# Performance work log

Hardware: AMD Instinct MI355X
Metric: run time of the kernel (lower is better)

Reference implementation:

```python
import jax, jax.numpy as jnp
import numpy as np

DIM = 512
HEADS = 8
DHEAD = DIM // 8          # 64
INNER = HEADS * DHEAD     # 512
M_LANDMARKS = 256
PINV_ITERS = 6
KSZ = 33                  # residual depthwise conv kernel (default)


def setup_inputs() -> dict:
    key = jax.random.key(0)
    ks = jax.random.split(key, 5)
    B, N = 1, 16384
    s = DIM ** -0.5
    return {
        "x": jax.random.normal(ks[0], (B, N, DIM), jnp.float32),
        "norm_w": jnp.ones((DIM,), jnp.float32),
        "norm_b": jnp.zeros((DIM,), jnp.float32),
        "w_qkv": jax.random.normal(ks[1], (3 * INNER, DIM), jnp.float32) * s,   # Linear(dim, 3*inner, bias=False)
        "w_out": jax.random.normal(ks[2], (DIM, INNER), jnp.float32) * s,        # Linear(inner, dim)
        "b_out": jnp.zeros((DIM,), jnp.float32),
        "conv_w": jax.random.normal(ks[3], (HEADS, 1, KSZ, 1), jnp.float32) * 0.1,  # depthwise Conv2d(h,h,(33,1),groups=h)
    }


def _layernorm(x, w, b, eps=1e-5):
    mu = x.mean(-1, keepdims=True)
    var = ((x - mu) ** 2).mean(-1, keepdims=True)
    return (x - mu) * jax.lax.rsqrt(var + eps) * w + b


def _moore_penrose_pinv(a, iters):
    # a: [B, H, m, m]; matches lucidrains moore_penrose_iter_pinv (global max over col/row sums)
    abs_a = jnp.abs(a)
    col = abs_a.sum(-1).max()
    row = abs_a.sum(-2).max()
    z = jnp.swapaxes(a, -1, -2) / (col * row)
    I = jnp.eye(a.shape[-1], dtype=a.dtype)
    for _ in range(iters):
        az = a @ z
        z = 0.25 * z @ (13 * I - az @ (15 * I - az @ (7 * I - az)))
    return z


def _nystrom_attention(h, w_qkv, w_out, b_out, conv_w):
    B, N, _ = h.shape
    qkv = h @ w_qkv.T                          # [B, N, 3*inner]
    q, k, v = jnp.split(qkv, 3, axis=-1)

    def heads(t):
        return t.reshape(B, N, HEADS, DHEAD).transpose(0, 2, 1, 3)  # [B, H, N, d]
    q = heads(q) * (DHEAD ** -0.5)
    k = heads(k)
    v = heads(v)

    # landmark pooling: mean over contiguous groups of size l = N / m
    l = N // M_LANDMARKS
    q_l = q.reshape(B, HEADS, M_LANDMARKS, l, DHEAD).mean(3)   # [B, H, m, d]
    k_l = k.reshape(B, HEADS, M_LANDMARKS, l, DHEAD).mean(3)

    attn1 = jax.nn.softmax(jnp.einsum('bhnd,bhmd->bhnm', q, k_l), axis=-1)      # [B,H,N,m]
    attn2 = jax.nn.softmax(jnp.einsum('bhid,bhjd->bhij', q_l, k_l), axis=-1)    # [B,H,m,m]
    attn3 = jax.nn.softmax(jnp.einsum('bhmd,bhnd->bhmn', q_l, k), axis=-1)      # [B,H,m,N]

    attn2_inv = _moore_penrose_pinv(attn2, PINV_ITERS)
    out = attn1 @ (attn2_inv @ (attn3 @ v))                                     # [B,H,N,d]

    # residual depthwise conv along sequence dim (kernel 33x1, groups=HEADS, no bias)
    conv = jax.lax.conv_general_dilated(
        v, conv_w, window_strides=(1, 1),
        padding=((KSZ // 2, KSZ // 2), (0, 0)),
        dimension_numbers=('NCHW', 'OIHW', 'NCHW'),
        feature_group_count=HEADS)
    out = out + conv

    out = out.transpose(0, 2, 1, 3).reshape(B, N, INNER)
    return out @ w_out.T + b_out


def reference(x, norm_w, norm_b, w_qkv, w_out, b_out, conv_w):
    h = _layernorm(x, norm_w, norm_b)
    return x + _nystrom_attention(h, w_qkv, w_out, b_out, conv_w)
```

## Files before the change

### kernel.cpp

```cpp
#include <hip/hip_runtime.h>
#include <hip/hip_bf16.h>


typedef __attribute__((ext_vector_type(8))) short bf16x8;
typedef __attribute__((ext_vector_type(4))) float f32x4;

#define MFMA16(A, B, C) __builtin_amdgcn_mfma_f32_16x16x32_bf16(A, B, C, 0, 0, 0)
#define GLD16(g, l) __builtin_amdgcn_global_load_lds( \
    (const __attribute__((address_space(1))) void*)(g), \
    (__attribute__((address_space(3))) void*)(l), 16, 0, 0)

static __device__ __forceinline__ unsigned short f2b(float f) {
  __hip_bfloat16 h = __float2bfloat16(f);
  return *reinterpret_cast<unsigned short*>(&h);
}
static __device__ __forceinline__ float b2f(unsigned short u) {
  return __uint_as_float(((unsigned)u) << 16);
}

#define FMA16(ACC, AV, BV) do { \
  ACC[0][0] += AV.x*BV.x; ACC[0][1] += AV.x*BV.y; ACC[0][2] += AV.x*BV.z; ACC[0][3] += AV.x*BV.w; \
  ACC[1][0] += AV.y*BV.x; ACC[1][1] += AV.y*BV.y; ACC[1][2] += AV.y*BV.z; ACC[1][3] += AV.y*BV.w; \
  ACC[2][0] += AV.z*BV.x; ACC[2][1] += AV.z*BV.y; ACC[2][2] += AV.z*BV.z; ACC[2][3] += AV.z*BV.w; \
  ACC[3][0] += AV.w*BV.x; ACC[3][1] += AV.w*BV.y; ACC[3][2] += AV.w*BV.z; ACC[3][3] += AV.w*BV.w; \
} while (0)

__global__ __launch_bounds__(128) void k_ln(const float* __restrict__ x,
    const float* __restrict__ w, const float* __restrict__ b, unsigned short* __restrict__ h) {
  const int row = blockIdx.x;
  const int t = threadIdx.x;
  const float4 xv = ((const float4*)(x + (size_t)row * 512))[t];
  float s  = xv.x + xv.y + xv.z + xv.w;
  float sq = xv.x*xv.x + xv.y*xv.y + xv.z*xv.z + xv.w*xv.w;
  #pragma unroll
  for (int o = 32; o > 0; o >>= 1) {
    s  += __shfl_down(s, o, 64);
    sq += __shfl_down(sq, o, 64);
  }
  __shared__ float ls[2], lq[2];
  if ((t & 63) == 0) { ls[t >> 6] = s; lq[t >> 6] = sq; }
  __syncthreads();
  s = ls[0] + ls[1]; sq = lq[0] + lq[1];
  const float mean = s * (1.0f / 512.0f);
  const float var  = sq * (1.0f / 512.0f) - mean * mean;
  const float rstd = rsqrtf(var + 1e-5f);
  const float4 wv = ((const float4*)w)[t];
  const float4 bv = ((const float4*)b)[t];
  ushort4 hv;
  hv.x = f2b((xv.x - mean) * rstd * wv.x + bv.x);
  hv.y = f2b((xv.y - mean) * rstd * wv.y + bv.y);
  hv.z = f2b((xv.z - mean) * rstd * wv.z + bv.z);
  hv.w = f2b((xv.w - mean) * rstd * wv.w + bv.w);
  ((ushort4*)(h + (size_t)row * 512))[t] = hv;
}

__global__ __launch_bounds__(256) void k_cvt(const float* __restrict__ src,
    unsigned short* __restrict__ dst, int n4) {
  const int i = blockIdx.x * 256 + threadIdx.x;
  if (i < n4) {
    const float4 f = ((const float4*)src)[i];
    ushort4 u;
    u.x = f2b(f.x); u.y = f2b(f.y); u.z = f2b(f.z); u.w = f2b(f.w);
    ((ushort4*)dst)[i] = u;
  }
}

__device__ __forceinline__ void stage_tile(const unsigned short* __restrict__ A,
    const unsigned short* __restrict__ B, unsigned short* lds,
    int m0, int n0, int k0, int tid) {
  #pragma unroll
  for (int c = 0; c < 2; ++c) {
    const int s = c * 512 + tid;
    const int grow = ((s >> 6) << 4) | (s & 15);
    const int chunk = (s >> 4) & 3;
    GLD16(A + (size_t)(m0 + grow) * 512 + k0 + chunk * 8, lds + s * 8);
    GLD16(B + (size_t)(n0 + grow) * 512 + k0 + chunk * 8, lds + 8192 + s * 8);
  }
}

__device__ __forceinline__ void compute_tile(const unsigned short* lds,
    f32x4 (&acc)[8][4], int wr, int wc, int quad, int l15) {
  bf16x8 a[8], b[4];
  #pragma unroll
  for (int i = 0; i < 8; ++i)
    a[i] = *(const bf16x8*)(lds + (size_t)((wr * 8 + i) * 64 + quad * 16 + l15) * 8);
  #pragma unroll
  for (int j = 0; j < 4; ++j)
    b[j] = *(const bf16x8*)(lds + 8192 + (size_t)((wc * 4 + j) * 64 + quad * 16 + l15) * 8);
  __builtin_amdgcn_s_setprio(1);
  #pragma unroll
  for (int i = 0; i < 8; ++i)
    #pragma unroll
    for (int j = 0; j < 4; ++j)
      acc[i][j] = MFMA16(a[i], b[j], acc[i][j]);
  __builtin_amdgcn_s_setprio(0);
}

#define GEMM256_PIPELINE(Aptr, Bptr, M0, N0)                                 \
  f32x4 acc[8][4];                                                           \
  _Pragma("unroll")                                                          \
  for (int i = 0; i < 8; ++i)                                                \
    _Pragma("unroll")                                                        \
    for (int j = 0; j < 4; ++j) acc[i][j] = (f32x4){0.f, 0.f, 0.f, 0.f};     \
  stage_tile(Aptr, Bptr, lds, M0, N0, 0, tid);                               \
  asm volatile("" ::: "memory");                                             \
  stage_tile(Aptr, Bptr, lds + 16384, M0, N0, 32, tid);                      \
  asm volatile("s_waitcnt vmcnt(4)" ::: "memory");                           \
  __builtin_amdgcn_s_barrier();                                              \
  {                                                                          \
    int cb = 0, sb = 2;                                                      \
    for (int t = 0; t < 14; ++t) {                                           \
      stage_tile(Aptr, Bptr, lds + sb * 16384, M0, N0, (t + 2) * 32, tid);   \
      compute_tile(lds + cb * 16384, acc, wr, wc, quad, l15);                \
      asm volatile("s_waitcnt vmcnt(4)" ::: "memory");                       \
      __builtin_amdgcn_s_barrier();                                          \
      cb = (cb == 2) ? 0 : cb + 1;                                           \
      sb = (sb == 2) ? 0 : sb + 1;                                           \
    }                                                                        \
    compute_tile(lds + cb * 16384, acc, wr, wc, quad, l15);                  \
    cb = (cb == 2) ? 0 : cb + 1;                                             \
    asm volatile("s_waitcnt vmcnt(0)" ::: "memory");                         \
    __builtin_amdgcn_s_barrier();                                            \
    compute_tile(lds + cb * 16384, acc, wr, wc, quad, l15);                  \
  }

__global__ __launch_bounds__(512, 2) void k_qkv2(const unsigned short* __restrict__ A,
    const unsigned short* __restrict__ B,
    unsigned short* __restrict__ qb, unsigned short* __restrict__ kb,
    unsigned short* __restrict__ vb) {
  __shared__ unsigned short lds[49152];
  const int tid = threadIdx.x;
  const int lane = tid & 63, w = tid >> 6;
  const int wr = w >> 2, wc = w & 3;
  const int quad = lane >> 4, l15 = lane & 15;
  const int bid = blockIdx.x;
  const int swz = (bid & 7) * 48 + (bid >> 3);
  const int by = swz / 6, bx = swz - by * 6;
  const int m0 = by * 256, n0 = bx * 256;

  GEMM256_PIPELINE(A, B, m0, n0)

  const int part = n0 >> 9;
  const int head = ((n0 & 511) >> 6) + wc;
  unsigned short* dst = (part == 0) ? qb : (part == 1) ? kb : vb;
  const float scale = (part == 0) ? 0.125f : 1.0f;
  unsigned short* dp = dst + (size_t)head * 16384 * 64;
  #pragma unroll
  for (int i = 0; i < 8; ++i) {
    const int rowb = m0 + wr * 128 + i * 16 + quad * 4;
    #pragma unroll
    for (int j = 0; j < 4; ++j) {
      const int dd = j * 16 + l15;
      #pragma unroll
      for (int r = 0; r < 4; ++r)
        dp[(size_t)(rowb + r) * 64 + dd] = f2b(acc[i][j][r] * scale);
    }
  }
}

__global__ __launch_bounds__(512, 2) void k_out2(const unsigned short* __restrict__ A,
    const unsigned short* __restrict__ B, const float* __restrict__ bias,
    const float* __restrict__ xres, float* __restrict__ out) {
  __shared__ unsigned short lds[49152];
  const int tid = threadIdx.x;
  const int lane = tid & 63, w = tid >> 6;
  const int wr = w >> 2, wc = w & 3;
  const int quad = lane >> 4, l15 = lane & 15;
  const int bid = blockIdx.x;
  const int swz = (bid & 7) * 16 + (bid >> 3);
  const int by = swz >> 1, bx = swz & 1;
  const int m0 = by * 256, n0 = bx * 256;

  GEMM256_PIPELINE(A, B, m0, n0)

  #pragma unroll
  for (int j = 0; j < 4; ++j) {
    const int col = n0 + wc * 64 + j * 16 + l15;
    const float bv = bias[col];
    #pragma unroll
    for (int i = 0; i < 8; ++i) {
      const int rowb = m0 + wr * 128 + i * 16 + quad * 4;
      #pragma unroll
      for (int r = 0; r < 4; ++r) {
        const size_t idx = (size_t)(rowb + r) * 512 + col;
        out[idx] = acc[i][j][r] + bv + xres[idx];
      }
    }
  }
}

__global__ __launch_bounds__(256) void k_tr(const unsigned short* __restrict__ v,
    unsigned short* __restrict__ vt) {
  __shared__ unsigned short T[64][72];
  const int t = threadIdx.x;
  const int n0 = blockIdx.x * 64, h = blockIdx.y;
  const int n = t >> 2, sg = (t & 3) * 16;
  const unsigned short* p = v + ((size_t)(h * 16384 + n0 + n)) * 64 + sg;
  #pragma unroll
  for (int i = 0; i < 16; i += 4) {
    const ushort4 u = *(const ushort4*)(p + i);
    T[sg + i + 0][n] = u.x; T[sg + i + 1][n] = u.y;
    T[sg + i + 2][n] = u.z; T[sg + i + 3][n] = u.w;
  }
  __syncthreads();
  const int d = t >> 2, so = (t & 3) * 16;
  unsigned short* q = vt + ((size_t)(h * 64 + d)) * 16384 + n0 + so;
  #pragma unroll
  for (int i = 0; i < 16; i += 4) {
    ushort4 u;
    u.x = T[d][so + i]; u.y = T[d][so + i + 1];
    u.z = T[d][so + i + 2]; u.w = T[d][so + i + 3];
    *(ushort4*)(q + i) = u;
  }
}

__global__ __launch_bounds__(256) void k_landmark(const unsigned short* __restrict__ qb,
    const unsigned short* __restrict__ kb, float* __restrict__ qlf,
    unsigned short* __restrict__ qlb, float* __restrict__ klf,
    unsigned short* __restrict__ klb) {
  const int t = threadIdx.x, d = t & 63, grp = t >> 6;
  const int m = blockIdx.x, h = blockIdx.y;
  const unsigned short* src = blockIdx.z ? kb : qb;
  const unsigned short* p = src + ((size_t)h * 16384 + m * 64 + grp * 16) * 64 + d;
  float s = 0.f;
  #pragma unroll
  for (int i = 0; i < 16; ++i) s += b2f(p[(size_t)i * 64]);
  __shared__ float red[4][64];
  red[grp][d] = s;
  __syncthreads();
  if (t < 64) {
    float v = (red[0][d] + red[1][d]) + (red[2][d] + red[3][d]);
    v *= (1.0f / 64.0f);
    const size_t oi = ((size_t)h * 256 + m) * 64 + d;
    if (blockIdx.z == 0) { qlf[oi] = v; qlb[oi] = f2b(v); }
    else                 { klf[oi] = v; klb[oi] = f2b(v); }
  }
}

__global__ __launch_bounds__(256) void k_attn2(const float* __restrict__ ql,
    const float* __restrict__ kl, float* __restrict__ a2, unsigned short* __restrict__ a2b) {
  const int i = blockIdx.x, h = blockIdx.y, j = threadIdx.x;
  __shared__ float qrow[64];
  __shared__ float wred[4];
  __shared__ float wsum[4];
  if (j < 64) qrow[j] = ql[((size_t)h * 256 + i) * 64 + j];
  __syncthreads();
  const float* kr = kl + ((size_t)h * 256 + j) * 64;
  float s = 0.f;
  #pragma unroll 8
  for (int d = 0; d < 64; ++d) s += qrow[d] * kr[d];
  float mx = s;
  #pragma unroll
  for (int o2 = 32; o2 > 0; o2 >>= 1) mx = fmaxf(mx, __shfl_xor(mx, o2, 64));
  if ((j & 63) == 0) wred[j >> 6] = mx;
  __syncthreads();
  mx = fmaxf(fmaxf(wred[0], wred[1]), fmaxf(wred[2], wred[3]));
  const float e = __expf(s - mx);
  float sm = e;
  #pragma unroll
  for (int o2 = 32; o2 > 0; o2 >>= 1) sm += __shfl_xor(sm, o2, 64);
  if ((j & 63) == 0) wsum[j >> 6] = sm;
  __syncthreads();
  sm = wsum[0] + wsum[1] + wsum[2] + wsum[3];
  const float v = e / sm;
  const size_t idx = ((size_t)h * 256 + i) * 256 + j;
  a2[idx] = v;
  a2b[idx] = f2b(v);
}

__global__ __launch_bounds__(256) void k_colsum(const float* __restrict__ a2,
    float* __restrict__ cm) {
  const int h = blockIdx.x, j = threadIdx.x;
  const float* p = a2 + (size_t)h * 65536 + j;
  float s = 0.f;
  for (int i = 0; i < 256; ++i) s += p[(size_t)i * 256];
  float mx = s;
  #pragma unroll
  for (int o2 = 32; o2 > 0; o2 >>= 1) mx = fmaxf(mx, __shfl_xor(mx, o2, 64));
  __shared__ float wred[4];
  if ((j & 63) == 0) wred[j >> 6] = mx;
  __syncthreads();
  if (j == 0) cm[h] = fmaxf(fmaxf(wred[0], wred[1]), fmaxf(wred[2], wred[3]));
}

__global__ __launch_bounds__(256) void k_z0(const float* __restrict__ a2,
    const float* __restrict__ cm, unsigned short* __restrict__ z0b,
    unsigned short* __restrict__ z0t) {
  __shared__ float T[64][65];
  const int bi = blockIdx.x, bj = blockIdx.y, h = blockIdx.z;
  const int t = threadIdx.x;
  const int r = t >> 2, cseg = (t & 3) * 16;
  float g = cm[0];
  #pragma unroll
  for (int c = 1; c < 8; ++c) g = fmaxf(g, cm[c]);
  const float inv = 1.0f / g;
  const float* p = a2 + ((size_t)h * 256 + bj * 64 + r) * 256 + bi * 64 + cseg;
  unsigned short* qt = z0t + ((size_t)h * 256 + bj * 64 + r) * 256 + bi * 64 + cseg;
  #pragma unroll
  for (int i = 0; i < 16; i += 4) {
    const float4 f = *(const float4*)(p + i);
    T[cseg + i + 0][r] = f.x; T[cseg + i + 1][r] = f.y;
    T[cseg + i + 2][r] = f.z; T[cseg + i + 3][r] = f.w;
    ushort4 u;
    u.x = f2b(f.x * inv); u.y = f2b(f.y * inv);
    u.z = f2b(f.z * inv); u.w = f2b(f.w * inv);
    *(ushort4*)(qt + i) = u;
  }
  __syncthreads();
  unsigned short* qb_ = z0b + ((size_t)h * 256 + bi * 64 + r) * 256 + bj * 64 + cseg;
  #pragma unroll
  for (int i = 0; i < 16; i += 4) {
    ushort4 u;
    u.x = f2b(T[r][cseg + i] * inv);     u.y = f2b(T[r][cseg + i + 1] * inv);
    u.z = f2b(T[r][cseg + i + 2] * inv); u.w = f2b(T[r][cseg + i + 3] * inv);
    *(ushort4*)(qb_ + i) = u;
  }
}

__global__ __launch_bounds__(256) void k_pgemm(const unsigned short* __restrict__ A,
    const unsigned short* __restrict__ Bt, unsigned short* __restrict__ Cn,
    unsigned short* __restrict__ Ct, float* __restrict__ Cf,
    float alpha, float sdiag, int use_diag) {
  __shared__ unsigned short As[64 * 128];
  __shared__ unsigned short Bs[64 * 128];
  const int t = threadIdx.x;
  const int lane = t & 63, w = t >> 6;
  const int quad = lane >> 4, l15 = lane & 15;
  const int bn = blockIdx.x, bm = blockIdx.y, h = blockIdx.z;
  const size_t hs = (size_t)h * 65536;
  const unsigned short* Ap = A + hs + (size_t)(bm * 64) * 256;
  const unsigned short* Bp = Bt + hs + (size_t)(bn * 64) * 256;
  f32x4 acc[4];
  #pragma unroll
  for (int j = 0; j < 4; ++j) acc[j] = (f32x4){0.f, 0.f, 0.f, 0.f};
  for (int kh = 0; kh < 2; ++kh) {
    __syncthreads();
    #pragma unroll
    for (int c = 0; c < 4; ++c) {
      const int slot = c * 256 + t;
      const int row = slot >> 4, pc = slot & 15;
      const int lc = pc ^ (row & 7);
      GLD16(Ap + (size_t)row * 256 + kh * 128 + lc * 8, As + slot * 8);
      GLD16(Bp + (size_t)row * 256 + kh * 128 + lc * 8, Bs + slot * 8);
    }
    __syncthreads();
    #pragma unroll
    for (int kc = 0; kc < 4; ++kc) {
      const int arow = w * 16 + l15;
      const bf16x8 a = *(const bf16x8*)(As + arow * 128 + ((kc * 4 + quad) ^ (arow & 7)) * 8);
      #pragma unroll
      for (int j = 0; j < 4; ++j) {
        const int brow = j * 16 + l15;
        const bf16x8 b = *(const bf16x8*)(Bs + brow * 128 + ((kc * 4 + quad) ^ (brow & 7)) * 8);
        acc[j] = MFMA16(a, b, acc[j]);
      }
    }
  }
  const int row0 = bm * 64 + w * 16 + quad * 4;
  #pragma unroll
  for (int j = 0; j < 4; ++j) {
    const int col = bn * 64 + j * 16 + l15;
    float v[4];
    #pragma unroll
    for (int r = 0; r < 4; ++r) v[r] = acc[j][r] * alpha;
    if (Cn) {
      #pragma unroll
      for (int r = 0; r < 4; ++r) Cn[hs + (size_t)(row0 + r) * 256 + col] = f2b(v[r]);
    }
    if (Cf) {
      #pragma unroll
      for (int r = 0; r < 4; ++r) Cf[hs + (size_t)(row0 + r) * 256 + col] = v[r];
    }
    ushort4 u;
    float tv[4];
    #pragma unroll
    for (int r = 0; r < 4; ++r)
      tv[r] = use_diag ? ((col == row0 + r ? sdiag : 0.f) - v[r]) : v[r];
    u.x = f2b(tv[0]); u.y = f2b(tv[1]); u.z = f2b(tv[2]); u.w = f2b(tv[3]);
    *(ushort4*)(Ct + hs + (size_t)col * 256 + row0) = u;
  }
}

__global__ __launch_bounds__(256) void k_gemm256(const float* __restrict__ A,
    const float* __restrict__ B, float* __restrict__ C,
    int lda, int ldb, int ldc,
    unsigned long long sA, unsigned long long sB, unsigned long long sC,
    float alpha, float sdiag, int use_diag,
    const float* __restrict__ rs, unsigned long long sRS) {
  A += (size_t)blockIdx.z * sA;
  B += (size_t)blockIdx.z * sB;
  C += (size_t)blockIdx.z * sC;
  if (rs) rs += (size_t)blockIdx.z * sRS;
  __shared__ float As[16][68];
  __shared__ float Bs[16][68];
  const int t = threadIdx.x, tx = t & 15, ty = t >> 4;
  const int bn = blockIdx.x, bm = blockIdx.y;
  const int lr = t >> 2, lk = (t & 3) << 2;
  const int bkr = t >> 4, bnc = (t & 15) << 2;
  float acc[4][4] = {{0.f}};
  for (int k0 = 0; k0 < 256; k0 += 16) {
    float4 a4 = *(const float4*)(A + (size_t)(bm * 64 + lr) * lda + k0 + lk);
    float4 b4 = *(const float4*)(B + (size_t)(k0 + bkr) * ldb + bn * 64 + bnc);
    if (use_diag) {
      const int kg = k0 + bkr, ngb = bn * 64 + bnc;
      b4.x = (kg == ngb + 0 ? sdiag : 0.f) - b4.x;
      b4.y = (kg == ngb + 1 ? sdiag : 0.f) - b4.y;
      b4.z = (kg == ngb + 2 ? sdiag : 0.f) - b4.z;
      b4.w = (kg == ngb + 3 ? sdiag : 0.f) - b4.w;
    }
    if (rs) {
      const float rv = 1.0f / rs[k0 + bkr];
      b4.x *= rv; b4.y *= rv; b4.z *= rv; b4.w *= rv;
    }
    __syncthreads();
    As[lk+0][lr] = a4.x; As[lk+1][lr] = a4.y; As[lk+2][lr] = a4.z; As[lk+3][lr] = a4.w;
    *(float4*)&Bs[bkr][bnc] = b4;
    __syncthreads();
    #pragma unroll
    for (int kq = 0; kq < 16; ++kq) {
      const float4 av = *(const float4*)&As[kq][ty << 2];
      const float4 bv = *(const float4*)&Bs[kq][tx << 2];
      FMA16(acc, av, bv);
    }
  }
  #pragma unroll
  for (int ii = 0; ii < 4; ++ii)
    #pragma unroll
    for (int jj = 0; jj < 4; ++jj)
      C[(size_t)(bm * 64 + (ty << 2) + ii) * ldc + bn * 64 + (tx << 2) + jj] =
          alpha * acc[ii][jj];
}

__global__ __launch_bounds__(256) void k_trD(const float* __restrict__ D,
    unsigned short* __restrict__ dt) {
  __shared__ float T[64][65];
  const int t = threadIdx.x;
  const int mc = blockIdx.x, h = blockIdx.y;
  const int m = t >> 2, sg = (t & 3) * 16;
  const float* p = D + ((size_t)(h * 256 + mc * 64 + m)) * 64 + sg;
  #pragma unroll
  for (int i = 0; i < 16; i += 4) {
    const float4 f = *(const float4*)(p + i);
    T[sg + i + 0][m] = f.x; T[sg + i + 1][m] = f.y;
    T[sg + i + 2][m] = f.z; T[sg + i + 3][m] = f.w;
  }
  __syncthreads();
  const int d = t >> 2, so = (t & 3) * 16;
  unsigned short* q = dt + ((size_t)(h * 64 + d)) * 256 + mc * 64 + so;
  #pragma unroll
  for (int i = 0; i < 16; i += 4) {
    ushort4 u;
    u.x = f2b(T[d][so + i]);     u.y = f2b(T[d][so + i + 1]);
    u.z = f2b(T[d][so + i + 2]); u.w = f2b(T[d][so + i + 3]);
    *(ushort4*)(q + i) = u;
  }
}

__global__ __launch_bounds__(256) void k_w3_mfma(const unsigned short* __restrict__ qlb,
    const unsigned short* __restrict__ kb, const unsigned short* __restrict__ vt,
    float* __restrict__ W, float* __restrict__ lsum) {
  __shared__ unsigned short QLs[64 * 64];
  __shared__ unsigned short Ks [64 * 64];
  __shared__ unsigned short Vts[64 * 64];
  __shared__ unsigned short Ps [64 * 64];
  const int t = threadIdx.x;
  const int lane = t & 63, w = t >> 6;
  const int quad = lane >> 4, l15 = lane & 15;
  const int kc = blockIdx.x, mt = blockIdx.y, h = blockIdx.z;
  #pragma unroll
  for (int c = 0; c < 2; ++c) {
    const int slot = c * 256 + t;
    const int row = slot >> 3, pc = slot & 7, lc = pc ^ (row & 7);
    GLD16(qlb + ((size_t)(h * 256 + mt * 64 + row)) * 64 + lc * 8, QLs + slot * 8);
  }
  __syncthreads();
  const int arow = w * 16 + l15;
  const bf16x8 aq0 = *(const bf16x8*)(QLs + arow * 64 + ((quad    ) ^ (arow & 7)) * 8);
  const bf16x8 aq1 = *(const bf16x8*)(QLs + arow * 64 + ((quad + 4) ^ (arow & 7)) * 8);
  f32x4 wacc[4];
  #pragma unroll
  for (int dt = 0; dt < 4; ++dt) wacc[dt] = (f32x4){0.f, 0.f, 0.f, 0.f};
  float lacc[4] = {0.f, 0.f, 0.f, 0.f};
  for (int ss = 0; ss < 16; ++ss) {
    const int n0 = kc * 1024 + ss * 64;
    __syncthreads();
    #pragma unroll
    for (int c = 0; c < 2; ++c) {
      const int slot = c * 256 + t;
      const int row = slot >> 3, pc = slot & 7, lc = pc ^ (row & 7);
      GLD16(kb + ((size_t)(h * 16384 + n0 + row)) * 64 + lc * 8, Ks + slot * 8);
      GLD16(vt + ((size_t)(h * 64 + row)) * 16384 + n0 + lc * 8, Vts + slot * 8);
    }
    __syncthreads();
    f32x4 s[4];
    #pragma unroll
    for (int j = 0; j < 4; ++j) {
      s[j] = (f32x4){0.f, 0.f, 0.f, 0.f};
      const int brow = j * 16 + l15;
      const bf16x8 b0 = *(const bf16x8*)(Ks + brow * 64 + ((quad    ) ^ (brow & 7)) * 8);
      const bf16x8 b1 = *(const bf16x8*)(Ks + brow * 64 + ((quad + 4) ^ (brow & 7)) * 8);
      s[j] = MFMA16(aq0, b0, s[j]);
      s[j] = MFMA16(aq1, b1, s[j]);
    }
    #pragma unroll
    for (int j = 0; j < 4; ++j)
      #pragma unroll
      for (int r = 0; r < 4; ++r) {
        const float e = __expf(s[j][r]);
        lacc[r] += e;
        const int prow = w * 16 + quad * 4 + r, pcol = j * 16 + l15;
        Ps[prow * 64 + (((pcol >> 3) ^ (prow & 7)) << 3) + (pcol & 7)] = f2b(e);
      }
    __syncthreads();
    const bf16x8 ap0 = *(const bf16x8*)(Ps + arow * 64 + ((quad    ) ^ (arow & 7)) * 8);
    const bf16x8 ap1 = *(const bf16x8*)(Ps + arow * 64 + ((quad + 4) ^ (arow & 7)) * 8);
    #pragma unroll
    for (int dt = 0; dt < 4; ++dt) {
      const int brow = dt * 16 + l15;
      const bf16x8 b0 = *(const bf16x8*)(Vts + brow * 64 + ((quad    ) ^ (brow & 7)) * 8);
      const bf16x8 b1 = *(const bf16x8*)(Vts + brow * 64 + ((quad + 4) ^ (brow & 7)) * 8);
      wacc[dt] = MFMA16(ap0, b0, wacc[dt]);
      wacc[dt] = MFMA16(ap1, b1, wacc[dt]);
    }
  }
  #pragma unroll
  for (int dt = 0; dt < 4; ++dt)
    #pragma unroll
    for (int r = 0; r < 4; ++r)
      atomicAdd(&W[((size_t)(h * 256 + mt * 64 + w * 16 + quad * 4 + r)) * 64 + dt * 16 + l15],
                wacc[dt][r]);
  #pragma unroll
  for (int r = 0; r < 4; ++r) {
    #pragma unroll
    for (int msk = 1; msk < 16; msk <<= 1) lacc[r] += __shfl_xor(lacc[r], msk, 64);
    if (l15 == 0)
      atomicAdd(&lsum[h * 256 + mt * 64 + w * 16 + quad * 4 + r], lacc[r]);
  }
}

__global__ __launch_bounds__(256) void k_attn1_mfma(const unsigned short* __restrict__ qb,
    const unsigned short* __restrict__ klb, const unsigned short* __restrict__ dtb,
    const unsigned short* __restrict__ vt, const float* __restrict__ cw,
    unsigned short* __restrict__ o) {
  __shared__ unsigned short Wb[64 * 96];
  __shared__ unsigned short Ks[64 * 64];
  __shared__ unsigned short Ds[64 * 64];
  __shared__ unsigned short Ps[64 * 64];
  __shared__ float Wsm[33];
  const int t = threadIdx.x;
  const int lane = t & 63, w = t >> 6;
  const int quad = lane >> 4, l15 = lane & 15;
  const int bt = blockIdx.x, h = blockIdx.y;
  const int n0 = bt * 64;
  if (t < 33) Wsm[t] = cw[h * 33 + t];
  #pragma unroll
  for (int c = 0; c < 2; ++c) {
    const int slot = c * 256 + t;
    const int row = slot >> 3, pc = slot & 7, lc = pc ^ (row & 7);
    GLD16(qb + ((size_t)(h * 16384 + n0 + row)) * 64 + lc * 8, Wb + slot * 8);
  }
  __syncthreads();
  const int arow = w * 16 + l15;
  const bf16x8 aq0 = *(const bf16x8*)(Wb + arow * 64 + ((quad    ) ^ (arow & 7)) * 8);
  const bf16x8 aq1 = *(const bf16x8*)(Wb + arow * 64 + ((quad + 4) ^ (arow & 7)) * 8);
  __syncthreads();
  {
    const int n = t >> 2;
    const int gb = (t & 3) * 24;
    #pragma unroll
    for (int i = 0; i < 24; ++i) {
      const int g = gb + i;
      const int j = g - n;
      const int src = n0 - 16 + g;
      const float val = (j >= 0 && j <= 32 && src >= 0 && src < 16384) ? Wsm[j] : 0.f;
      Wb[n * 96 + (((g >> 3) ^ (n & 3)) << 3) + (g & 7)] = f2b(val);
    }
  }
  __syncthreads();
  f32x4 cacc[4];
  #pragma unroll
  for (int dt = 0; dt < 4; ++dt) cacc[dt] = (f32x4){0.f, 0.f, 0.f, 0.f};
  #pragma unroll
  for (int kcc = 0; kcc < 3; ++kcc) {
    const bf16x8 a = *(const bf16x8*)(Wb + arow * 96 + (((kcc * 4 + quad) ^ (arow & 3)) << 3));
    int off = n0 - 16 + kcc * 32 + quad * 8;
    off = off < 0 ? 0 : (off > 16376 ? 16376 : off);
    #pragma unroll
    for (int dt = 0; dt < 4; ++dt) {
      const bf16x8 b = *(const bf16x8*)(vt + ((size_t)(h * 64 + dt * 16 + l15)) * 16384 + off);
      cacc[dt] = MFMA16(a, b, cacc[dt]);
    }
  }
  f32x4 oacc[4];
  #pragma unroll
  for (int dt = 0; dt < 4; ++dt) oacc[dt] = (f32x4){0.f, 0.f, 0.f, 0.f};
  float lacc[4] = {0.f, 0.f, 0.f, 0.f};
  for (int mc = 0; mc < 4; ++mc) {
    const int m0 = mc * 64;
    __syncthreads();
    #pragma unroll
    for (int c = 0; c < 2; ++c) {
      const int slot = c * 256 + t;
      const int row = slot >> 3, pc = slot & 7, lc = pc ^ (row & 7);
      GLD16(klb + ((size_t)(h * 256 + m0 + row)) * 64 + lc * 8, Ks + slot * 8);
      GLD16(dtb + ((size_t)(h * 64 + row)) * 256 + m0 + lc * 8, Ds + slot * 8);
    }
    __syncthreads();
    f32x4 s[4];
    #pragma unroll
    for (int j = 0; j < 4; ++j) {
      s[j] = (f32x4){0.f, 0.f, 0.f, 0.f};
      const int brow = j * 16 + l15;
      const bf16x8 b0 = *(const bf16x8*)(Ks + brow * 64 + ((quad    ) ^ (brow & 7)) * 8);
      const bf16x8 b1 = *(const bf16x8*)(Ks + brow * 64 + ((quad + 4) ^ (brow & 7)) * 8);
      s[j] = MFMA16(aq0, b0, s[j]);
      s[j] = MFMA16(aq1, b1, s[j]);
    }
    #pragma unroll
    for (int j = 0; j < 4; ++j)
      #pragma unroll
      for (int r = 0; r < 4; ++r) {
        const float e = __expf(s[j][r]);
        lacc[r] += e;
        const int prow = w * 16 + quad * 4 + r, pcol = j * 16 + l15;
        Ps[prow * 64 + (((pcol >> 3) ^ (prow & 7)) << 3) + (pcol & 7)] = f2b(e);
      }
    __syncthreads();
    const bf16x8 ap0 = *(const bf16x8*)(Ps + arow * 64 + ((quad    ) ^ (arow & 7)) * 8);
    const bf16x8 ap1 = *(const bf16x8*)(Ps + arow * 64 + ((quad + 4) ^ (arow & 7)) * 8);
    #pragma unroll
    for (int dt = 0; dt < 4; ++dt) {
      const int brow = dt * 16 + l15;
      const bf16x8 b0 = *(const bf16x8*)(Ds + brow * 64 + ((quad    ) ^ (brow & 7)) * 8);
      const bf16x8 b1 = *(const bf16x8*)(Ds + brow * 64 + ((quad + 4) ^ (brow & 7)) * 8);
      oacc[dt] = MFMA16(ap0, b0, oacc[dt]);
      oacc[dt] = MFMA16(ap1, b1, oacc[dt]);
    }
  }
  #pragma unroll
  for (int r = 0; r < 4; ++r)
    #pragma unroll
    for (int msk = 1; msk < 16; msk <<= 1) lacc[r] += __shfl_xor(lacc[r], msk, 64);
  #pragma unroll
  for (int dt = 0; dt < 4; ++dt)
    #pragma unroll
    for (int r = 0; r < 4; ++r) {
      const float val = oacc[dt][r] / lacc[r] + cacc[dt][r];
      o[((size_t)(n0 + w * 16 + quad * 4 + r)) * 512 + h * 64 + dt * 16 + l15] = f2b(val);
    }
}

extern "C" void kernel_launch(void* const* d_in, const int* in_sizes, int n_in,
                              void* d_out, int out_size, void* d_ws, size_t ws_size,
                              hipStream_t stream) {
  const float* x      = (const float*)d_in[0];
  const float* norm_w = (const float*)d_in[1];
  const float* norm_b = (const float*)d_in[2];
  const float* w_qkv  = (const float*)d_in[3];
  const float* w_out  = (const float*)d_in[4];
  const float* b_out  = (const float*)d_in[5];
  const float* conv_w = (const float*)d_in[6];
  float* out = (float*)d_out;

  char* cur = (char*)d_ws;
  auto alloc = [&](size_t bytes) -> char* {
    char* p = cur;
    cur += (bytes + 255) & ~(size_t)255;
    return p;
  };
  const size_t NB = (size_t)16384 * 512;
  const size_t LM = (size_t)8 * 256 * 64;
  const size_t SQ = (size_t)8 * 256 * 256;

  unsigned short* h_b  = (unsigned short*)alloc(NB * 2);
  unsigned short* wq_b = (unsigned short*)alloc((size_t)1536 * 512 * 2);
  unsigned short* wo_b = (unsigned short*)alloc((size_t)512 * 512 * 2);
  unsigned short* qb   = (unsigned short*)alloc(NB * 2);
  unsigned short* kb   = (unsigned short*)alloc(NB * 2);
  unsigned short* vb   = (unsigned short*)alloc(NB * 2);
  unsigned short* vt   = (unsigned short*)alloc(NB * 2);
  float*          qlf  = (float*)alloc(LM * 4);
  float*          klf  = (float*)alloc(LM * 4);
  unsigned short* qlb  = (unsigned short*)alloc(LM * 2);
  unsigned short* klb  = (unsigned short*)alloc(LM * 2);
  float*          a2   = (float*)alloc(SQ * 4);
  unsigned short* a2b  = (unsigned short*)alloc(SQ * 2);
  unsigned short* z0b  = (unsigned short*)alloc(SQ * 2);
  unsigned short* z0t  = (unsigned short*)alloc(SQ * 2);
  unsigned short* Pn   = (unsigned short*)alloc(SQ * 2);
  unsigned short* Pt   = (unsigned short*)alloc(SQ * 2);
  unsigned short* Q1t  = (unsigned short*)alloc(SQ * 2);
  unsigned short* Q2t  = (unsigned short*)alloc(SQ * 2);
  unsigned short* zp0n = (unsigned short*)alloc(SQ * 2);
  unsigned short* zp0t = (unsigned short*)alloc(SQ * 2);
  unsigned short* zp1n = (unsigned short*)alloc(SQ * 2);
  unsigned short* zp1t = (unsigned short*)alloc(SQ * 2);
  float*          zf5  = (float*)alloc(SQ * 4);
  float*          zfin = (float*)alloc(SQ * 4);
  float*          Pp   = (float*)alloc(SQ * 4);
  float*          Q1   = (float*)alloc(SQ * 4);
  float*          Q2   = (float*)alloc(SQ * 4);
  float*          W    = (float*)alloc(LM * 4 + 2048 * 4);
  float*          lsum = W + LM;
  float*          D    = (float*)alloc(LM * 4);
  unsigned short* dtb  = (unsigned short*)alloc(LM * 2);
  float*          cm   = (float*)alloc(64 * 4);
  unsigned short* o_b  = (unsigned short*)alloc(NB * 2);

  hipMemsetAsync(W, 0, (LM + 2048) * sizeof(float), stream);
  k_ln<<<16384, 128, 0, stream>>>(x, norm_w, norm_b, h_b);
  k_cvt<<<768, 256, 0, stream>>>(w_qkv, wq_b, 196608);
  k_cvt<<<256, 256, 0, stream>>>(w_out, wo_b, 65536);
  k_qkv2<<<384, 512, 0, stream>>>(h_b, wq_b, qb, kb, vb);
  k_tr<<<dim3(256, 8), 256, 0, stream>>>(vb, vt);
  k_landmark<<<dim3(256, 8, 2), 256, 0, stream>>>(qb, kb, qlf, qlb, klf, klb);
  k_attn2<<<dim3(256, 8), 256, 0, stream>>>(qlf, klf, a2, a2b);
  k_colsum<<<8, 256, 0, stream>>>(a2, cm);
  k_z0<<<dim3(4, 4, 8), 256, 0, stream>>>(a2, cm, z0b, z0t);

  unsigned short* zan = z0b; unsigned short* zat = z0t;
  for (int it = 0; it < 5; ++it) {
    unsigned short* zbn = (it & 1) ? zp1n : zp0n;
    unsigned short* zbt = (it & 1) ? zp1t : zp0t;
    k_pgemm<<<dim3(4, 4, 8), 256, 0, stream>>>(a2b, zat, Pn, Pt, nullptr, 1.f, 7.f, 1);
    k_pgemm<<<dim3(4, 4, 8), 256, 0, stream>>>(Pn, Pt, nullptr, Q1t, nullptr, 1.f, 15.f, 1);
    k_pgemm<<<dim3(4, 4, 8), 256, 0, stream>>>(Pn, Q1t, nullptr, Q2t, nullptr, 1.f, 13.f, 1);
    k_pgemm<<<dim3(4, 4, 8), 256, 0, stream>>>(zan, Q2t, zbn, zbt,
        it == 4 ? zf5 : nullptr, 0.25f, 0.f, 0);
    zan = zbn; zat = zbt;
  }
  k_gemm256<<<dim3(4, 4, 8), 256, 0, stream>>>(a2, zf5, Pp, 256, 256, 256,
      65536ULL, 65536ULL, 65536ULL, 1.f, 0.f, 0, nullptr, 0ULL);
  k_gemm256<<<dim3(4, 4, 8), 256, 0, stream>>>(Pp, Pp, Q1, 256, 256, 256,
      65536ULL, 65536ULL, 65536ULL, 1.f, 7.f, 1, nullptr, 0ULL);
  k_gemm256<<<dim3(4, 4, 8), 256, 0, stream>>>(Pp, Q1, Q2, 256, 256, 256,
      65536ULL, 65536ULL, 65536ULL, 1.f, 15.f, 1, nullptr, 0ULL);
  k_gemm256<<<dim3(4, 4, 8), 256, 0, stream>>>(zf5, Q2, zfin, 256, 256, 256,
      65536ULL, 65536ULL, 65536ULL, 0.25f, 13.f, 1, nullptr, 0ULL);

  k_w3_mfma<<<dim3(16, 4, 8), 256, 0, stream>>>(qlb, kb, vt, W, lsum);
  k_gemm256<<<dim3(1, 4, 8), 256, 0, stream>>>(zfin, W, D, 256, 64, 64,
      65536ULL, 16384ULL, 16384ULL, 1.f, 0.f, 0, lsum, 256ULL);
  k_trD<<<dim3(4, 8), 256, 0, stream>>>(D, dtb);
  k_attn1_mfma<<<dim3(256, 8), 256, 0, stream>>>(qb, klb, dtb, vt, conv_w, o_b);
  k_out2<<<128, 512, 0, stream>>>(o_b, wo_b, b_out, x, out);
}
```

Measured before the change: 464.1 us.

## Fuse pinv iterations into one cooperative kernel, rework QKV and output GEMMs

The roughly 26 small launches of the Newton–Schulz pseudo-inverse chain, the final D GEMM and the D transpose are merged into one cooperative kernel that uses grid.sync between steps. This removes per-launch overhead and writes the transposed bf16 D directly. The QKV GEMM pipeline drops from triple to double LDS buffering so 4 blocks can fit per CU, with an extra barrier each step. The output projection is replaced by a simpler 128x128-tile MFMA kernel with no software pipelining, which may be slower per tile.

```diff
diff --git a/kernel.cpp b/kernel.cpp
--- a/kernel.cpp
+++ b/kernel.cpp
@@ -1,5 +1,8 @@
 #include <hip/hip_runtime.h>
 #include <hip/hip_bf16.h>
+#include <hip/hip_cooperative_groups.h>
+
+namespace cg = cooperative_groups;
 
 
 typedef __attribute__((ext_vector_type(8))) short bf16x8;
@@ -107,28 +110,25 @@
   stage_tile(Aptr, Bptr, lds + 16384, M0, N0, 32, tid);                      \
   asm volatile("s_waitcnt vmcnt(4)" ::: "memory");                           \
   __builtin_amdgcn_s_barrier();                                              \
-  {                                                                          \
-    int cb = 0, sb = 2;                                                      \
-    for (int t = 0; t < 14; ++t) {                                           \
-      stage_tile(Aptr, Bptr, lds + sb * 16384, M0, N0, (t + 2) * 32, tid);   \
-      compute_tile(lds + cb * 16384, acc, wr, wc, quad, l15);                \
-      asm volatile("s_waitcnt vmcnt(4)" ::: "memory");                       \
-      __builtin_amdgcn_s_barrier();                                          \
-      cb = (cb == 2) ? 0 : cb + 1;                                           \
-      sb = (sb == 2) ? 0 : sb + 1;                                           \
-    }                                                                        \
-    compute_tile(lds + cb * 16384, acc, wr, wc, quad, l15);                  \
-    cb = (cb == 2) ? 0 : cb + 1;                                             \
-    asm volatile("s_waitcnt vmcnt(0)" ::: "memory");                         \
+  for (int t = 0; t < 14; ++t) {                                             \
+    compute_tile(lds + (t & 1) * 16384, acc, wr, wc, quad, l15);             \
+    asm volatile("" ::: "memory");                                           \
+    __builtin_amdgcn_s_barrier();       \
+    asm volatile("" ::: "memory");                                           \
+    stage_tile(Aptr, Bptr, lds + (t & 1) * 16384, M0, N0, (t + 2) * 32, tid);\
+    asm volatile("s_waitcnt vmcnt(4)" ::: "memory");    \
     __builtin_amdgcn_s_barrier();                                            \
-    compute_tile(lds + cb * 16384, acc, wr, wc, quad, l15);                  \
-  }
-
-__global__ __launch_bounds__(512, 2) void k_qkv2(const unsigned short* __restrict__ A,
+  }                                                                          \
+  compute_tile(lds, acc, wr, wc, quad, l15);             \
+  asm volatile("s_waitcnt vmcnt(0)" ::: "memory");                           \
+  __builtin_amdgcn_s_barrier();                                              \
+  compute_tile(lds + 16384, acc, wr, wc, quad, l15);
+
+__global__ __launch_bounds__(512, 4) void k_qkv2(const unsigned short* __restrict__ A,
     const unsigned short* __restrict__ B,
     unsigned short* __restrict__ qb, unsigned short* __restrict__ kb,
     unsigned short* __restrict__ vb) {
-  __shared__ unsigned short lds[49152];
+  __shared__ __align__(16) unsigned short lds[32768];
   const int tid = threadIdx.x;
   const int lane = tid & 63, w = tid >> 6;
   const int wr = w >> 2, wc = w & 3;
@@ -158,35 +158,54 @@
   }
 }
 
-__global__ __launch_bounds__(512, 2) void k_out2(const unsigned short* __restrict__ A,
+__global__ __launch_bounds__(256) void k_out_mfma(const unsigned short* __restrict__ A,
     const unsigned short* __restrict__ B, const float* __restrict__ bias,
     const float* __restrict__ xres, float* __restrict__ out) {
-  __shared__ unsigned short lds[49152];
-  const int tid = threadIdx.x;
-  const int lane = tid & 63, w = tid >> 6;
-  const int wr = w >> 2, wc = w & 3;
+  __shared__ unsigned short As[128 * 32];
+  __shared__ unsigned short Bs[128 * 32];
+  const int t = threadIdx.x;
+  const int lane = t & 63, w = t >> 6;
   const int quad = lane >> 4, l15 = lane & 15;
-  const int bid = blockIdx.x;
-  const int swz = (bid & 7) * 16 + (bid >> 3);
-  const int by = swz >> 1, bx = swz & 1;
-  const int m0 = by * 256, n0 = bx * 256;
-
-  GEMM256_PIPELINE(A, B, m0, n0)
-
-  #pragma unroll
-  for (int j = 0; j < 4; ++j) {
-    const int col = n0 + wc * 64 + j * 16 + l15;
-    const float bv = bias[col];
-    #pragma unroll
-    for (int i = 0; i < 8; ++i) {
-      const int rowb = m0 + wr * 128 + i * 16 + quad * 4;
+  const int wm = (w >> 1) * 64, wn = (w & 1) * 64;
+  const int m0 = blockIdx.y * 128, n0 = blockIdx.x * 128;
+  f32x4 acc[4][4];
+  #pragma unroll
+  for (int i = 0; i < 4; ++i)
+    #pragma unroll
+    for (int j = 0; j < 4; ++j) acc[i][j] = (f32x4){0.f, 0.f, 0.f, 0.f};
+  for (int k0 = 0; k0 < 512; k0 += 32) {
+    __syncthreads();
+    #pragma unroll
+    for (int c = 0; c < 2; ++c) {
+      const int slot = c * 256 + t;
+      const int row = slot >> 2, seg = slot & 3;
+      GLD16(A + (size_t)(m0 + row) * 512 + k0 + seg * 8, As + slot * 8);
+      GLD16(B + (size_t)(n0 + row) * 512 + k0 + seg * 8, Bs + slot * 8);
+    }
+    __syncthreads();
+    bf16x8 a[4], b[4];
+    #pragma unroll
+    for (int i = 0; i < 4; ++i)
+      a[i] = *(const bf16x8*)(As + (wm + i * 16 + l15) * 32 + quad * 8);
+    #pragma unroll
+    for (int j = 0; j < 4; ++j)
+      b[j] = *(const bf16x8*)(Bs + (wn + j * 16 + l15) * 32 + quad * 8);
+    #pragma unroll
+    for (int i = 0; i < 4; ++i)
+      #pragma unroll
+      for (int j = 0; j < 4; ++j)
+        acc[i][j] = MFMA16(a[i], b[j], acc[i][j]);
+  }
+  #pragma unroll
+  for (int i = 0; i < 4; ++i)
+    #pragma unroll
+    for (int j = 0; j < 4; ++j)
       #pragma unroll
       for (int r = 0; r < 4; ++r) {
-        const size_t idx = (size_t)(rowb + r) * 512 + col;
-        out[idx] = acc[i][j][r] + bv + xres[idx];
+        const int row = m0 + wm + i * 16 + quad * 4 + r;
+        const int col = n0 + wn + j * 16 + l15;
+        out[(size_t)row * 512 + col] = acc[i][j][r] + bias[col] + xres[(size_t)row * 512 + col];
       }
-    }
-  }
 }
 
 __global__ __launch_bounds__(256) void k_tr(const unsigned short* __restrict__ v,
@@ -317,16 +336,14 @@
   }
 }
 
-__global__ __launch_bounds__(256) void k_pgemm(const unsigned short* __restrict__ A,
+__device__ __forceinline__ void pg_step(const unsigned short* __restrict__ A,
     const unsigned short* __restrict__ Bt, unsigned short* __restrict__ Cn,
     unsigned short* __restrict__ Ct, float* __restrict__ Cf,
-    float alpha, float sdiag, int use_diag) {
-  __shared__ unsigned short As[64 * 128];
-  __shared__ unsigned short Bs[64 * 128];
+    float alpha, float sdiag, int use_diag,
+    unsigned short* As, unsigned short* Bs, int bn, int bm, int h) {
   const int t = threadIdx.x;
   const int lane = t & 63, w = t >> 6;
   const int quad = lane >> 4, l15 = lane & 15;
-  const int bn = blockIdx.x, bm = blockIdx.y, h = blockIdx.z;
   const size_t hs = (size_t)h * 65536;
   const unsigned short* Ap = A + hs + (size_t)(bm * 64) * 256;
   const unsigned short* Bp = Bt + hs + (size_t)(bn * 64) * 256;
@@ -381,26 +398,18 @@
   }
 }
 
-__global__ __launch_bounds__(256) void k_gemm256(const float* __restrict__ A,
+__device__ __forceinline__ void g256_step(const float* __restrict__ A,
     const float* __restrict__ B, float* __restrict__ C,
-    int lda, int ldb, int ldc,
-    unsigned long long sA, unsigned long long sB, unsigned long long sC,
     float alpha, float sdiag, int use_diag,
-    const float* __restrict__ rs, unsigned long long sRS) {
-  A += (size_t)blockIdx.z * sA;
-  B += (size_t)blockIdx.z * sB;
-  C += (size_t)blockIdx.z * sC;
-  if (rs) rs += (size_t)blockIdx.z * sRS;
-  __shared__ float As[16][68];
-  __shared__ float Bs[16][68];
+    float* Asf, float* Bsf, int bn, int bm, int h) {
+  A += (size_t)h * 65536; B += (size_t)h * 65536; C += (size_t)h * 65536;
   const int t = threadIdx.x, tx = t & 15, ty = t >> 4;
-  const int bn = blockIdx.x, bm = blockIdx.y;
   const int lr = t >> 2, lk = (t & 3) << 2;
   const int bkr = t >> 4, bnc = (t & 15) << 2;
   float acc[4][4] = {{0.f}};
   for (int k0 = 0; k0 < 256; k0 += 16) {
-    float4 a4 = *(const float4*)(A + (size_t)(bm * 64 + lr) * lda + k0 + lk);
-    float4 b4 = *(const float4*)(B + (size_t)(k0 + bkr) * ldb + bn * 64 + bnc);
+    float4 a4 = *(const float4*)(A + (size_t)(bm * 64 + lr) * 256 + k0 + lk);
+    float4 b4 = *(const float4*)(B + (size_t)(k0 + bkr) * 256 + bn * 64 + bnc);
     if (use_diag) {
       const int kg = k0 + bkr, ngb = bn * 64 + bnc;
       b4.x = (kg == ngb + 0 ? sdiag : 0.f) - b4.x;
@@ -408,18 +417,15 @@
       b4.z = (kg == ngb + 2 ? sdiag : 0.f) - b4.z;
       b4.w = (kg == ngb + 3 ? sdiag : 0.f) - b4.w;
     }
-    if (rs) {
-      const float rv = 1.0f / rs[k0 + bkr];
-      b4.x *= rv; b4.y *= rv; b4.z *= rv; b4.w *= rv;
-    }
-    __syncthreads();
-    As[lk+0][lr] = a4.x; As[lk+1][lr] = a4.y; As[lk+2][lr] = a4.z; As[lk+3][lr] = a4.w;
-    *(float4*)&Bs[bkr][bnc] = b4;
+    __syncthreads();
+    Asf[(lk + 0) * 68 + lr] = a4.x; Asf[(lk + 1) * 68 + lr] = a4.y;
+    Asf[(lk + 2) * 68 + lr] = a4.z; Asf[(lk + 3) * 68 + lr] = a4.w;
+    *(float4*)&Bsf[bkr * 68 + bnc] = b4;
     __syncthreads();
     #pragma unroll
     for (int kq = 0; kq < 16; ++kq) {
-      const float4 av = *(const float4*)&As[kq][ty << 2];
-      const float4 bv = *(const float4*)&Bs[kq][tx << 2];
+      const float4 av = *(const float4*)&Asf[kq * 68 + (ty << 2)];
+      const float4 bv = *(const float4*)&Bsf[kq * 68 + (tx << 2)];
       FMA16(acc, av, bv);
     }
   }
@@ -427,33 +433,84 @@
   for (int ii = 0; ii < 4; ++ii)
     #pragma unroll
     for (int jj = 0; jj < 4; ++jj)
-      C[(size_t)(bm * 64 + (ty << 2) + ii) * ldc + bn * 64 + (tx << 2) + jj] =
+      C[(size_t)(bm * 64 + (ty << 2) + ii) * 256 + bn * 64 + (tx << 2) + jj] =
           alpha * acc[ii][jj];
 }
 
-__global__ __launch_bounds__(256) void k_trD(const float* __restrict__ D,
-    unsigned short* __restrict__ dt) {
-  __shared__ float T[64][65];
-  const int t = threadIdx.x;
-  const int mc = blockIdx.x, h = blockIdx.y;
-  const int m = t >> 2, sg = (t & 3) * 16;
-  const float* p = D + ((size_t)(h * 256 + mc * 64 + m)) * 64 + sg;
-  #pragma unroll
-  for (int i = 0; i < 16; i += 4) {
-    const float4 f = *(const float4*)(p + i);
-    T[sg + i + 0][m] = f.x; T[sg + i + 1][m] = f.y;
-    T[sg + i + 2][m] = f.z; T[sg + i + 3][m] = f.w;
-  }
-  __syncthreads();
-  const int d = t >> 2, so = (t & 3) * 16;
-  unsigned short* q = dt + ((size_t)(h * 64 + d)) * 256 + mc * 64 + so;
-  #pragma unroll
-  for (int i = 0; i < 16; i += 4) {
-    ushort4 u;
-    u.x = f2b(T[d][so + i]);     u.y = f2b(T[d][so + i + 1]);
-    u.z = f2b(T[d][so + i + 2]); u.w = f2b(T[d][so + i + 3]);
-    *(ushort4*)(q + i) = u;
-  }
+__device__ __forceinline__ void g256_D(const float* __restrict__ A,
+    const float* __restrict__ B, const float* __restrict__ rs,
+    unsigned short* __restrict__ dtb, float* Asf, float* Bsf, int bm, int h) {
+  A += (size_t)h * 65536;
+  B += (size_t)h * 16384;
+  rs += (size_t)h * 256;
+  const int t = threadIdx.x, tx = t & 15, ty = t >> 4;
+  const int lr = t >> 2, lk = (t & 3) << 2;
+  const int bkr = t >> 4, bnc = (t & 15) << 2;
+  float acc[4][4] = {{0.f}};
+  for (int k0 = 0; k0 < 256; k0 += 16) {
+    float4 a4 = *(const float4*)(A + (size_t)(bm * 64 + lr) * 256 + k0 + lk);
+    float4 b4 = *(const float4*)(B + (size_t)(k0 + bkr) * 64 + bnc);
+    const float rv = 1.0f / rs[k0 + bkr];
+    b4.x *= rv; b4.y *= rv; b4.z *= rv; b4.w *= rv;
+    __syncthreads();
+    Asf[(lk + 0) * 68 + lr] = a4.x; Asf[(lk + 1) * 68 + lr] = a4.y;
+    Asf[(lk + 2) * 68 + lr] = a4.z; Asf[(lk + 3) * 68 + lr] = a4.w;
+    *(float4*)&Bsf[bkr * 68 + bnc] = b4;
+    __syncthreads();
+    #pragma unroll
+    for (int kq = 0; kq < 16; ++kq) {
+      const float4 av = *(const float4*)&Asf[kq * 68 + (ty << 2)];
+      const float4 bv = *(const float4*)&Bsf[kq * 68 + (tx << 2)];
+      FMA16(acc, av, bv);
+    }
+  }
+  #pragma unroll
+  for (int ii = 0; ii < 4; ++ii)
+    #pragma unroll
+    for (int jj = 0; jj < 4; ++jj)
+      dtb[(size_t)(h * 64 + (tx << 2) + jj) * 256 + bm * 64 + (ty << 2) + ii] =
+          f2b(acc[ii][jj]);
+}
+
+__global__ __launch_bounds__(256) void k_pinv(
+    const unsigned short* a2b, const float* a2,
+    const unsigned short* z0b, const unsigned short* z0t,
+    unsigned short* zp0n, unsigned short* zp0t,
+    unsigned short* zp1n, unsigned short* zp1t,
+    unsigned short* Pn, unsigned short* Pt,
+    unsigned short* Q1t, unsigned short* Q2t,
+    float* zf5, float* Pp, float* Q1, float* Q2, float* zfin,
+    const float* W, const float* lsum, unsigned short* dtb) {
+  cg::grid_group grid = cg::this_grid();
+  __shared__ __align__(16) unsigned short As[64 * 128];
+  __shared__ __align__(16) unsigned short Bs[64 * 128];
+  const int bid = blockIdx.x;
+  const int bn = bid & 3, bm = (bid >> 2) & 3, h = bid >> 4;
+
+  const unsigned short* zan = z0b;
+  const unsigned short* zat = z0t;
+  #pragma unroll 1
+  for (int it = 0; it < 5; ++it) {
+    unsigned short* zbn = (it & 1) ? zp1n : zp0n;
+    unsigned short* zbt = (it & 1) ? zp1t : zp0t;
+    pg_step(a2b, zat, Pn, Pt, nullptr, 1.f, 7.f, 1, As, Bs, bn, bm, h);
+    grid.sync();
+    pg_step(Pn, Pt, nullptr, Q1t, nullptr, 1.f, 15.f, 1, As, Bs, bn, bm, h);
+    grid.sync();
+    pg_step(Pn, Q1t, nullptr, Q2t, nullptr, 1.f, 13.f, 1, As, Bs, bn, bm, h);
+    grid.sync();
+    pg_step(zan, Q2t, zbn, zbt, (it == 4) ? zf5 : nullptr, 0.25f, 0.f, 0,
+            As, Bs, bn, bm, h);
+    grid.sync();
+    zan = zbn; zat = zbt;
+  }
+  float* Asf = (float*)As;
+  float* Bsf = (float*)Bs;
+  g256_step(a2, zf5, Pp, 1.f, 0.f, 0, Asf, Bsf, bn, bm, h);  grid.sync();
+  g256_step(Pp, Pp, Q1, 1.f, 7.f, 1, Asf, Bsf, bn, bm, h);   grid.sync();
+  g256_step(Pp, Q1, Q2, 1.f, 15.f, 1, Asf, Bsf, bn, bm, h);  grid.sync();
+  g256_step(zf5, Q2, zfin, 0.25f, 13.f, 1, Asf, Bsf, bn, bm, h); grid.sync();
+  if (bn == 0) g256_D(zfin, W, lsum, dtb, Asf, Bsf, bm, h);
 }
 
 __global__ __launch_bounds__(256) void k_w3_mfma(const unsigned short* __restrict__ qlb,
@@ -706,6 +763,7 @@
   unsigned short* dtb  = (unsigned short*)alloc(LM * 2);
   float*          cm   = (float*)alloc(64 * 4);
   unsigned short* o_b  = (unsigned short*)alloc(NB * 2);
+  (void)D;
 
   hipMemsetAsync(W, 0, (LM + 2048) * sizeof(float), stream);
   k_ln<<<16384, 128, 0, stream>>>(x, norm_w, norm_b, h_b);
@@ -717,31 +775,19 @@
   k_attn2<<<dim3(256, 8), 256, 0, stream>>>(qlf, klf, a2, a2b);
   k_colsum<<<8, 256, 0, stream>>>(a2, cm);
   k_z0<<<dim3(4, 4, 8), 256, 0, stream>>>(a2, cm, z0b, z0t);
-
-  unsigned short* zan = z0b; unsigned short* zat = z0t;
-  for (int it = 0; it < 5; ++it) {
-    unsigned short* zbn = (it & 1) ? zp1n : zp0n;
-    unsigned short* zbt = (it & 1) ? zp1t : zp0t;
-    k_pgemm<<<dim3(4, 4, 8), 256, 0, stream>>>(a2b, zat, Pn, Pt, nullptr, 1.f, 7.f, 1);
-    k_pgemm<<<dim3(4, 4, 8), 256, 0, stream>>>(Pn, Pt, nullptr, Q1t, nullptr, 1.f, 15.f, 1);
-    k_pgemm<<<dim3(4, 4, 8), 256, 0, stream>>>(Pn, Q1t, nullptr, Q2t, nullptr, 1.f, 13.f, 1);
-    k_pgemm<<<dim3(4, 4, 8), 256, 0, stream>>>(zan, Q2t, zbn, zbt,
-        it == 4 ? zf5 : nullptr, 0.25f, 0.f, 0);
-    zan = zbn; zat = zbt;
-  }
-  k_gemm256<<<dim3(4, 4, 8), 256, 0, stream>>>(a2, zf5, Pp, 256, 256, 256,
-      65536ULL, 65536ULL, 65536ULL, 1.f, 0.f, 0, nullptr, 0ULL);
-  k_gemm256<<<dim3(4, 4, 8), 256, 0, stream>>>(Pp, Pp, Q1, 256, 256, 256,
-      65536ULL, 65536ULL, 65536ULL, 1.f, 7.f, 1, nullptr, 0ULL);
-  k_gemm256<<<dim3(4, 4, 8), 256, 0, stream>>>(Pp, Q1, Q2, 256, 256, 256,
-      65536ULL, 65536ULL, 65536ULL, 1.f, 15.f, 1, nullptr, 0ULL);
-  k_gemm256<<<dim3(4, 4, 8), 256, 0, stream>>>(zf5, Q2, zfin, 256, 256, 256,
-      65536ULL, 65536ULL, 65536ULL, 0.25f, 13.f, 1, nullptr, 0ULL);
-
   k_w3_mfma<<<dim3(16, 4, 8), 256, 0, stream>>>(qlb, kb, vt, W, lsum);
-  k_gemm256<<<dim3(1, 4, 8), 256, 0, stream>>>(zfin, W, D, 256, 64, 64,
-      65536ULL, 16384ULL, 16384ULL, 1.f, 0.f, 0, lsum, 256ULL);
-  k_trD<<<dim3(4, 8), 256, 0, stream>>>(D, dtb);
+
+  {
+    void* pargs[] = {
+      (void*)&a2b, (void*)&a2, (void*)&z0b, (void*)&z0t,
+      (void*)&zp0n, (void*)&zp0t, (void*)&zp1n, (void*)&zp1t,
+      (void*)&Pn, (void*)&Pt, (void*)&Q1t, (void*)&Q2t,
+      (void*)&zf5, (void*)&Pp, (void*)&Q1, (void*)&Q2, (void*)&zfin,
+      (void*)&W, (void*)&lsum, (void*)&dtb
+    };
+    hipLaunchCooperativeKernel((void*)k_pinv, dim3(128), dim3(256), pargs, 0, stream);
+  }
+
   k_attn1_mfma<<<dim3(256, 8), 256, 0, stream>>>(qb, klb, dtb, vt, conv_w, o_b);
-  k_out2<<<128, 512, 0, stream>>>(o_b, wo_b, b_out, x, out);
-}
+  k_out_mfma<<<dim3(4, 128), 256, 0, stream>>>(o_b, wo_b, b_out, x, out);
+}
```

Result: slower. 1.088 ms (+134.5%).
